# Optimization experiments

Measured on AMD Instinct MI355X. Metric: run time of the kernel, lower is better.

The kernel has to match this reference:

```python
import jax, jax.numpy as jnp
import numpy as np

# ---- module config (matches init_kwargs; defaults: theta_am_is_mod_index=False,
# theta_fm_is_mod_index=True) ----
SR = 44100
N_SAMPLES = 65536
B = 256
F0_MIN, F0_MAX = 32.7, 523.25
AM_MIN, AM_MAX = 0.5, 8.0
FM_MIN, FM_MAX = 0.5, 8.0
MI_AM_MIN, MI_AM_MAX = 0.0, 1.0
MI_FM_MIN, MI_FM_MAX = 0.0, 1.0
TWO_PI = 2.0 * np.pi


def _log2(x):
    return float(np.log2(x))


def setup_inputs() -> dict:
    key = jax.random.key(0)
    ks = jax.random.split(key, 8)
    u = lambda k: jax.random.uniform(k, (B,), dtype=jnp.float32)
    return {
        "theta_am_0to1": u(ks[0]),
        "theta_fm_0to1": u(ks[1]),
        "phase": u(ks[2]),      # scaled by 2*pi inside reference
        "phase_am": u(ks[3]),
        "phase_fm": u(ks[4]),
        "u_am_mi": u(ks[5]),    # -> mi_am   (theta_am_is_mod_index=False)
        "u_fm_hz": u(ks[6]),    # -> fm_hz   (theta_fm_is_mod_index=True)
        "u_f0_hz": u(ks[7]),    # -> f0_hz
    }


def reference(theta_am_0to1, theta_fm_0to1, phase, phase_am, phase_fm,
              u_am_mi, u_fm_hz, u_f0_hz):
    t = (jnp.arange(N_SAMPLES, dtype=jnp.float32) / SR)[None, :]  # [1, N]

    # theta_am_is_mod_index=False: theta_am is the AM carrier rate (log-uniform),
    # mod index drawn uniformly in [MI_AM_MIN, MI_AM_MAX].
    am_lo, am_hi = _log2(AM_MIN), _log2(AM_MAX)
    am_hz = jnp.exp2(theta_am_0to1 * (am_hi - am_lo) + am_lo)       # [B]
    mi_am = u_am_mi * (MI_AM_MAX - MI_AM_MIN) + MI_AM_MIN           # [B]

    # theta_fm_is_mod_index=True: theta_fm is the FM mod index, rate is random
    # log-uniform in [FM_MIN, FM_MAX].
    mi_fm = theta_fm_0to1 * (MI_FM_MAX - MI_FM_MIN) + MI_FM_MIN     # [B]
    fm_lo, fm_hi = _log2(FM_MIN), _log2(FM_MAX)
    fm_hz = jnp.exp2(u_fm_hz * (fm_hi - fm_lo) + fm_lo)             # [B]

    f0_lo, f0_hi = _log2(F0_MIN), _log2(F0_MAX)
    f0_hz = jnp.exp2(u_f0_hz * (f0_hi - f0_lo) + f0_lo)             # [B]

    am_sig = jnp.sin(TWO_PI * am_hz[:, None] * t + TWO_PI * phase_am[:, None]) * mi_am[:, None]  # [B,N]
    fm_sig = jnp.sin(TWO_PI * fm_hz[:, None] * t + TWO_PI * phase_fm[:, None]) * mi_fm[:, None]  # [B,N]

    # f0_hz + fm_sig * f0_hz (exactly the torch math; when mi_fm==0, fm_sig==0)
    f0_inst = f0_hz[:, None] * (1.0 + fm_sig)                        # [B,N]
    arg = jnp.cumsum(TWO_PI * f0_inst / SR, axis=1) + TWO_PI * phase[:, None]
    x = 0.5 * jnp.sin(arg)
    x = x * (1.0 + am_sig)  # x + am_sig * x
    return x[:, None, :]    # [B, 1, N]
```

## Files before the change

kernel.cpp:

```cpp
#include <hip/hip_runtime.h>
#include <math.h>

#define SR_D        44100.0
#define N_SAMPLES   65536
#define BVOICES     256
#define TWO_PI_F    6.28318530717958647692f
#define TWO_PI_D    6.28318530717958647692528676655900577

#define TPB 256
#define SPT 16
#define SPB (TPB*SPT)
#define BLOCKS_PER_ROW (N_SAMPLES / SPB)

struct VoiceD {
    double Cc;
    double c1;
    double th0rev;
    double fmrev;
    double pam0;
    double amrev;
};
struct VoiceF {
    float c1f;
    float fmrevf;
    float K4f;
    float miamf;
    float amrevf;
    float pad0, pad1, pad2;
};

__device__ VoiceD g_vd[BVOICES];
__device__ VoiceF g_vf[BVOICES];

__global__ void amfm_setup_kernel(const float* __restrict__ th_am,
                                  const float* __restrict__ th_fm,
                                  const float* __restrict__ ph,
                                  const float* __restrict__ ph_am,
                                  const float* __restrict__ ph_fm,
                                  const float* __restrict__ u_am_mi,
                                  const float* __restrict__ u_fm_hz,
                                  const float* __restrict__ u_f0_hz) {
    int i = threadIdx.x;
    if (i >= BVOICES) return;

    float am_hz = exp2f(th_am[i] * 4.0f - 1.0f);
    float mi_am = u_am_mi[i];
    float mi_fm = th_fm[i];
    float fm_hz = exp2f(u_fm_hz[i] * 4.0f - 1.0f);
    const double l2lo = log2(32.7);
    const double l2hi = log2(523.25);
    float f0_hz = exp2f(u_f0_hz[i] * (float)(l2hi - l2lo) + (float)l2lo);

    double c1  = (double)f0_hz / SR_D;
    double h   = M_PI * (double)fm_hz / SR_D;
    double K4  = c1 * (double)mi_fm / (2.0 * sin(h));
    double a   = TWO_PI_D * (double)ph_fm[i];
    double Cc  = (double)ph[i] + K4 * cos(a - h);

    VoiceD d;
    d.Cc     = Cc;
    d.c1     = c1;
    d.th0rev = (a + h) / TWO_PI_D;
    d.fmrev  = (double)fm_hz / SR_D;
    d.pam0   = (double)ph_am[i];
    d.amrev  = (double)am_hz / SR_D;
    g_vd[i] = d;

    VoiceF f;
    f.c1f    = (float)c1;
    f.fmrevf = (float)d.fmrev;
    f.K4f    = (float)K4;
    f.miamf  = mi_am;
    f.amrevf = (float)d.amrev;
    f.pad0 = f.pad1 = f.pad2 = 0.0f;
    g_vf[i] = f;
}

__global__ void __launch_bounds__(TPB)
amfm_synth_kernel(float* __restrict__ out) {
    const int bid  = blockIdx.x;
    const int row  = bid >> 4;
    const int col0 = (bid & (BLOCKS_PER_ROW - 1)) * SPB;
    const int n0   = col0 + threadIdx.x * SPT;

    const VoiceD d = g_vd[row];
    const VoiceF f = g_vf[row];

    double db = d.Cc + d.c1 * (double)(n0 + 1);
    float carb = (float)(db - floor(db));
    double tb = d.th0rev + d.fmrev * (double)n0;
    float thb = (float)(tb - floor(tb));
    double ab = d.pam0 + d.amrev * (double)n0;
    float amb = (float)(ab - floor(ab));

    float res[SPT];
#pragma unroll
    for (int k = 0; k < SPT; ++k) {
        float lr = fmaf(f.c1f, (float)k, carb);
        float th = fmaf(f.fmrevf, (float)k, thb);
        th -= floorf(th);
        float cv = __cosf(TWO_PI_F * th);
        float ar = fmaf(-f.K4f, cv, lr);
        ar -= floorf(ar);
        float s = __sinf(TWO_PI_F * ar);
        float am = fmaf(f.amrevf, (float)k, amb);
        am -= floorf(am);
        float av = __sinf(TWO_PI_F * am);
        res[k] = 0.5f * s * fmaf(f.miamf, av, 1.0f);
    }

    float* op = out + (size_t)row * N_SAMPLES + n0;
#pragma unroll
    for (int j = 0; j < SPT / 4; ++j) {
        reinterpret_cast<float4*>(op)[j] =
            make_float4(res[4*j], res[4*j+1], res[4*j+2], res[4*j+3]);
    }
}

extern "C" void kernel_launch(void* const* d_in, const int* in_sizes, int n_in,
                              void* d_out, int out_size, void* d_ws, size_t ws_size,
                              hipStream_t stream) {
    const float* th_am  = (const float*)d_in[0];
    const float* th_fm  = (const float*)d_in[1];
    const float* ph     = (const float*)d_in[2];
    const float* ph_am  = (const float*)d_in[3];
    const float* ph_fm  = (const float*)d_in[4];
    const float* u_am   = (const float*)d_in[5];
    const float* u_fm   = (const float*)d_in[6];
    const float* u_f0   = (const float*)d_in[7];
    float* out = (float*)d_out;

    amfm_setup_kernel<<<1, BVOICES, 0, stream>>>(th_am, th_fm, ph, ph_am, ph_fm,
                                                 u_am, u_fm, u_f0);
    const int nblocks = BVOICES * BLOCKS_PER_ROW;
    amfm_synth_kernel<<<nblocks, TPB, 0, stream>>>(out);
}
```

Before: 104.8 us.

## Interleave per-thread sample groups for coalesced float4 stores

Each thread now handles four groups of four contiguous samples spaced a block-width apart, instead of sixteen contiguous samples. Consecutive threads therefore write adjacent float4s, so each store instruction is coalesced across the wavefront. Phases are advanced between groups with precomputed fractional increments, and the 0.5 factor is folded into the AM mod index. Accumulating float phase increments adds a small precision risk.

```diff
diff --git a/kernel.cpp b/kernel.cpp
--- a/kernel.cpp
+++ b/kernel.cpp
@@ -8,8 +8,9 @@
 #define TWO_PI_D    6.28318530717958647692528676655900577
 
 #define TPB 256
-#define SPT 16
-#define SPB (TPB*SPT)
+#define GROUPS 4
+#define GROUP_STRIDE (TPB * 4)
+#define SPB (GROUP_STRIDE * GROUPS)
 #define BLOCKS_PER_ROW (N_SAMPLES / SPB)
 
 struct VoiceD {
@@ -23,14 +24,18 @@
 struct VoiceF {
     float c1f;
     float fmrevf;
+    float amrevf;
     float K4f;
-    float miamf;
-    float amrevf;
-    float pad0, pad1, pad2;
+    float halfmi;
+    float c1k;
+    float fmk;
+    float amk;
 };
 
 __device__ VoiceD g_vd[BVOICES];
 __device__ VoiceF g_vf[BVOICES];
+
+__device__ __forceinline__ float fractf(float x) { return x - floorf(x); }
 
 __global__ void amfm_setup_kernel(const float* __restrict__ th_am,
                                   const float* __restrict__ th_fm,
@@ -69,10 +74,13 @@
     VoiceF f;
     f.c1f    = (float)c1;
     f.fmrevf = (float)d.fmrev;
+    f.amrevf = (float)d.amrev;
     f.K4f    = (float)K4;
-    f.miamf  = mi_am;
-    f.amrevf = (float)d.amrev;
-    f.pad0 = f.pad1 = f.pad2 = 0.0f;
+    f.halfmi = 0.5f * mi_am;
+    double g = (double)GROUP_STRIDE;
+    f.c1k    = (float)(g * c1      - floor(g * c1));
+    f.fmk    = (float)(g * d.fmrev - floor(g * d.fmrev));
+    f.amk    = (float)(g * d.amrev - floor(g * d.amrev));
     g_vf[i] = f;
 }
 
@@ -81,7 +89,8 @@
     const int bid  = blockIdx.x;
     const int row  = bid >> 4;
     const int col0 = (bid & (BLOCKS_PER_ROW - 1)) * SPB;
-    const int n0   = col0 + threadIdx.x * SPT;
+    const int t4   = threadIdx.x * 4;
+    const int n0   = col0 + t4;
 
     const VoiceD d = g_vd[row];
     const VoiceF f = g_vf[row];
@@ -93,27 +102,28 @@
     double ab = d.pam0 + d.amrev * (double)n0;
     float amb = (float)(ab - floor(ab));
 
-    float res[SPT];
+    float* op = out + (size_t)row * N_SAMPLES + n0;
+
 #pragma unroll
-    for (int k = 0; k < SPT; ++k) {
-        float lr = fmaf(f.c1f, (float)k, carb);
-        float th = fmaf(f.fmrevf, (float)k, thb);
-        th -= floorf(th);
-        float cv = __cosf(TWO_PI_F * th);
-        float ar = fmaf(-f.K4f, cv, lr);
-        ar -= floorf(ar);
-        float s = __sinf(TWO_PI_F * ar);
-        float am = fmaf(f.amrevf, (float)k, amb);
-        am -= floorf(am);
-        float av = __sinf(TWO_PI_F * am);
-        res[k] = 0.5f * s * fmaf(f.miamf, av, 1.0f);
-    }
-
-    float* op = out + (size_t)row * N_SAMPLES + n0;
+    for (int j = 0; j < GROUPS; ++j) {
+        float r[4];
 #pragma unroll
-    for (int j = 0; j < SPT / 4; ++j) {
-        reinterpret_cast<float4*>(op)[j] =
-            make_float4(res[4*j], res[4*j+1], res[4*j+2], res[4*j+3]);
+        for (int k = 0; k < 4; ++k) {
+            const float kk = (float)k;
+            float th = fractf(fmaf(f.fmrevf, kk, thb));
+            float cv = __cosf(TWO_PI_F * th);
+            float ar = fmaf(-f.K4f, cv, fmaf(f.c1f, kk, carb));
+            ar = fractf(ar);
+            float s = __sinf(TWO_PI_F * ar);
+            float am = fractf(fmaf(f.amrevf, kk, amb));
+            float av = __sinf(TWO_PI_F * am);
+            r[k] = s * fmaf(f.halfmi, av, 0.5f);
+        }
+        reinterpret_cast<float4*>(op + j * GROUP_STRIDE)[0] =
+            make_float4(r[0], r[1], r[2], r[3]);
+        carb = fractf(carb + f.c1k);
+        thb  = fractf(thb + f.fmk);
+        amb  = fractf(amb + f.amk);
     }
 }
 
```

Result: faster. 95.94 us (-8.5%).
